# Kernel optimization log

Measured on AMD Instinct MI355X. Metric: run time of the kernel, lower is better.

The kernel has to match this reference:

```python
import jax, jax.numpy as jnp
import numpy as np
import jax.scipy.special as jsp

N_RESERVOIR = 8192
N_INPUT = 64
N_LAYERS = 3
INPUT_SCALE = 0.4
RES_SCALE = 0.9
BIAS_SCALE = 0.1
ALPHA = 1.0  # activation_fn_args = (1.0,)
N_HADAMARD = 1 << int(np.ceil(np.log2(N_INPUT + N_RESERVOIR)))  # 16384
N_PADDING = N_HADAMARD - N_RESERVOIR - N_INPUT
BATCH = 512


def fwht(x):
    """Fast Walsh-Hadamard transform along last axis. x: [B, n], n a power of 2."""
    B, n = x.shape
    h = 1
    while h < n:
        x = x.reshape(B, n // (2 * h), 2, h)
        a = x[:, :, 0, :]
        b = x[:, :, 1, :]
        x = jnp.concatenate([a + b, a - b], axis=-1).reshape(B, n)
        h *= 2
    return x


def leaky_erf(x, state, alpha):
    return (1.0 - alpha) * state + alpha * jsp.erf(x)


def setup_inputs() -> dict:
    key = jax.random.key(0)
    k1, k2, k3, k4 = jax.random.split(key, 4)
    state = jax.random.normal(k1, (BATCH, N_RESERVOIR), dtype=jnp.float32)
    inputs = jax.random.normal(k2, (BATCH, N_INPUT), dtype=jnp.float32)
    bias = BIAS_SCALE * jax.random.normal(k3, (N_RESERVOIR,), dtype=jnp.float32)
    # structured-transform diagonals: random Rademacher signs, one per layer
    diag = jnp.where(jax.random.uniform(k4, (N_LAYERS, N_HADAMARD)) < 0.5, -1.0, 1.0).astype(jnp.float32)
    return {"state": state, "inputs": inputs, "bias": bias, "diag": diag}


def reference(state, inputs, bias, diag):
    B = state.shape[0]
    pad = jnp.zeros((B, N_PADDING), dtype=state.dtype)
    X = jnp.concatenate([RES_SCALE * state, INPUT_SCALE * inputs, pad], axis=1)  # [B, N_HADAMARD]
    for l in range(N_LAYERS):
        X = fwht(X * diag[l])
    z = X[:, :N_RESERVOIR] / N_HADAMARD + bias
    return leaky_erf(z, state, ALPHA)
```

## Files before the change

kernel.cpp:

```cpp
#include <hip/hip_runtime.h>
#include <math.h>

#define NH    16384
#define NRES  8192
#define NINP  64
#define BATCH 512

typedef float v2f __attribute__((ext_vector_type(2)));

__device__ __forceinline__ constexpr int gfold(int v) {
    return ((v >> 5) & 7) ^ ((v >> 8) & 7) ^ ((v >> 11) & 7);
}
__device__ __forceinline__ constexpr int physf(int v) {
    return v ^ (gfold(v) << 2);
}

template <int T>
__device__ __forceinline__ void pstage(v2f X[32]) {
#pragma unroll
    for (int p = 0; p < 32; ++p) {
        if (!(p & T)) {
            v2f A = X[p], B = X[p | T];
            X[p]     = A + B;
            X[p | T] = A - B;
        }
    }
}
__device__ __forceinline__ void vstage0(v2f X[32]) {
#pragma unroll
    for (int p = 0; p < 32; ++p) {
        float a = X[p].x, b = X[p].y;
        X[p].x = a + b;
        X[p].y = a - b;
    }
}

template <int CTRL>
__device__ __forceinline__ float dppf(float v) {
    return __builtin_bit_cast(float,
        __builtin_amdgcn_update_dpp(0, __builtin_bit_cast(int, v), CTRL, 0xF, 0xF, true));
}
template <int CTRL>
__device__ __forceinline__ void dpp_swap(float A, float B, bool odd, float& oA, float& oB) {
    float dA = dppf<CTRL>(A), dB = dppf<CTRL>(B);
    oA = odd ? dB : A;
    oB = odd ? B  : dA;
}
__device__ __forceinline__ void pl16_swap(float& a, float& b) {
    asm("v_permlane16_swap_b32 %0, %1" : "+v"(a), "+v"(b));
}
__device__ __forceinline__ void pl32_swap(float& a, float& b) {
    asm("v_permlane32_swap_b32 %0, %1" : "+v"(a), "+v"(b));
}

__device__ __forceinline__ void shuffle_exchange(v2f X[32], bool odd0, bool odd1) {
#pragma unroll
    for (int p = 0; p < 32; ++p) if (!(p & 2)) {
        float a0, a1, b0, b1;
        dpp_swap<0xB1>(X[p].x, X[p | 2].x, odd0, a0, b0);
        dpp_swap<0xB1>(X[p].y, X[p | 2].y, odd0, a1, b1);
        X[p] = (v2f){a0, a1}; X[p | 2] = (v2f){b0, b1};
    }
#pragma unroll
    for (int p = 0; p < 32; ++p) if (!(p & 4)) {
        float a0, a1, b0, b1;
        dpp_swap<0x4E>(X[p].x, X[p | 4].x, odd1, a0, b0);
        dpp_swap<0x4E>(X[p].y, X[p | 4].y, odd1, a1, b1);
        X[p] = (v2f){a0, a1}; X[p | 4] = (v2f){b0, b1};
    }
#pragma unroll
    for (int p = 0; p < 32; ++p) if (!(p & 8)) {
        float a = X[p].x, b = X[p | 8].x; pl16_swap(a, b); X[p].x = a; X[p | 8].x = b;
        float c = X[p].y, d = X[p | 8].y; pl16_swap(c, d); X[p].y = c; X[p | 8].y = d;
    }
#pragma unroll
    for (int p = 0; p < 32; ++p) if (!(p & 16)) {
        float a = X[p].x, b = X[p | 16].x; pl32_swap(a, b); X[p].x = a; X[p | 16].x = b;
        float c = X[p].y, d = X[p | 16].y; pl32_swap(c, d); X[p].y = c; X[p | 16].y = d;
    }
}

#define WRX(Q, SH) do { _Pragma("unroll") \
    for (int j = 0; j < 16; ++j) \
        lds4[(unsigned)((Q) ^ physf(j << (SH))) >> 2] = \
            make_float4(X[2*j].x, X[2*j].y, X[2*j+1].x, X[2*j+1].y); } while (0)

#define RDX(Q, SH) do { _Pragma("unroll") \
    for (int j = 0; j < 16; ++j) { \
        float4 v = lds4[(unsigned)((Q) ^ physf(j << (SH))) >> 2]; \
        X[2*j]   = (v2f){v.x, v.y}; \
        X[2*j+1] = (v2f){v.z, v.w}; } } while (0)

#define DIAG_MUL(BASEPTR, SH) do { \
    _Pragma("unroll") for (int h = 0; h < 2; ++h) { \
        float4 dv[8]; \
        _Pragma("unroll") for (int k = 0; k < 8; ++k) \
            dv[k] = *(const float4*)((BASEPTR) + ((h * 8 + k) << (SH))); \
        _Pragma("unroll") for (int k = 0; k < 8; ++k) { \
            const int j = h * 8 + k; \
            X[2*j]   *= (v2f){dv[k].x, dv[k].y}; \
            X[2*j+1] *= (v2f){dv[k].z, dv[k].w}; \
        } \
    } } while (0)

__device__ __forceinline__ float erf_fast(float z) {
    float p = z * z;
    float u = z * fmaf(p, 0.10090f, 1.1283793f);
    float e = __builtin_amdgcn_exp2f(u * 2.8853902f);
    float r = __builtin_amdgcn_rcpf(e + 1.0f);
    return fmaf(-2.0f, r, 1.0f);
}


__global__ __launch_bounds__(256, 2) void st_kernel(
    const float* __restrict__ state, const float* __restrict__ inputs,
    const float* __restrict__ bias,  const float* __restrict__ diag,
    float* __restrict__ out)
{
    __shared__ float4 lds4[NH / 4];
    const int t = threadIdx.x;
    const int r = blockIdx.x;
    const int l = t & 63, w = t >> 6;
    const int l01 = l & 3, l23 = (l >> 2) & 3, l45 = (l >> 4) & 3;
    const bool odd0 = (l & 1), odd1 = (l & 2);

    const int bA = (w << 12) | (l23 << 10) | (l45 << 8) | (l01 << 6);
    const int bB = (w << 12) | (l23 << 10) | (l45 << 4) | (l01 << 2);
    const int bC = (w << 8)  | (l23 << 6)  | (l45 << 4) | (l01 << 2);
    const int bD = (l45 << 12) | (l01 << 10) | (w << 8) | (l23 << 6);

    v2f X[32];

    if (t < 128) {
        const float* srow = state + (size_t)r * NRES + bA;
        const float* d0   = diag + bA;
#pragma unroll
        for (int h = 0; h < 2; ++h) {
            float4 sv[8], dv[8];
#pragma unroll
            for (int k = 0; k < 8; ++k) {
                sv[k] = *(const float4*)(srow + 4 * (h * 8 + k));
                dv[k] = *(const float4*)(d0   + 4 * (h * 8 + k));
            }
#pragma unroll
            for (int k = 0; k < 8; ++k) {
                const int j = h * 8 + k;
                X[2*j]   = (v2f){0.9f * sv[k].x * dv[k].x, 0.9f * sv[k].y * dv[k].y};
                X[2*j+1] = (v2f){0.9f * sv[k].z * dv[k].z, 0.9f * sv[k].w * dv[k].w};
            }
        }
    } else if (t == 128) {
        const float* irow = inputs + r * NINP;
        const float* d0   = diag + NRES;
#pragma unroll
        for (int j = 0; j < 16; ++j) {
            float4 v = *(const float4*)(irow + 4 * j);
            float4 d = *(const float4*)(d0 + 4 * j);
            X[2*j]   = (v2f){0.4f * v.x * d.x, 0.4f * v.y * d.y};
            X[2*j+1] = (v2f){0.4f * v.z * d.z, 0.4f * v.w * d.w};
        }
    } else {
#pragma unroll
        for (int p = 0; p < 32; ++p) X[p] = (v2f){0.f, 0.f};
    }

    vstage0(X); pstage<1>(X); pstage<2>(X);
    pstage<4>(X); pstage<8>(X); pstage<16>(X);

    shuffle_exchange(X, odd0, odd1);
    pstage<2>(X); pstage<4>(X); pstage<8>(X); pstage<16>(X);

    { const int Q = physf(bB); WRX(Q, 6); }
    __syncthreads();
    { const int Q = physf(bC); RDX(Q, 10); }
    pstage<2>(X); pstage<4>(X); pstage<8>(X); pstage<16>(X);
    DIAG_MUL(diag + NH + bC, 10);
    vstage0(X); pstage<1>(X);
    pstage<2>(X); pstage<4>(X); pstage<8>(X); pstage<16>(X);

    shuffle_exchange(X, odd0, odd1);
    pstage<2>(X); pstage<4>(X); pstage<8>(X); pstage<16>(X);

    __syncthreads();
    { const int Q = physf(bD); WRX(Q, 2); }
    __syncthreads();
    { const int Q = physf(bB); RDX(Q, 6); }
    pstage<2>(X); pstage<4>(X); pstage<8>(X); pstage<16>(X);
    DIAG_MUL(diag + 2 * NH + bB, 6);
    vstage0(X); pstage<1>(X);
    pstage<2>(X); pstage<4>(X); pstage<8>(X); pstage<16>(X);

    shuffle_exchange(X, odd0, odd1);
    pstage<2>(X); pstage<4>(X); pstage<8>(X); pstage<16>(X);

    __syncthreads();
    { const int Q = physf(bA); WRX(Q, 2); }
    __syncthreads();
    { const int Q = physf(bC); RDX(Q, 10); }
    pstage<2>(X); pstage<4>(X); pstage<8>(X); pstage<16>(X);

    {
        float* orow = out + (size_t)r * NRES;
        const float inv = 1.0f / (float)NH;
#pragma unroll
        for (int j = 0; j < 8; ++j) {
            float4 b = *(const float4*)(bias + bC + (j << 10));
            float4 o;
            o.x = erf_fast(fmaf(X[2*j].x,   inv, b.x));
            o.y = erf_fast(fmaf(X[2*j].y,   inv, b.y));
            o.z = erf_fast(fmaf(X[2*j+1].x, inv, b.z));
            o.w = erf_fast(fmaf(X[2*j+1].y, inv, b.w));
            *(float4*)(orow + bC + (j << 10)) = o;
        }
    }
}

extern "C" void kernel_launch(void* const* d_in, const int* in_sizes, int n_in,
                              void* d_out, int out_size, void* d_ws, size_t ws_size,
                              hipStream_t stream) {
    (void)in_sizes; (void)n_in; (void)out_size; (void)d_ws; (void)ws_size;
    const float* state  = (const float*)d_in[0];
    const float* inputs = (const float*)d_in[1];
    const float* bias   = (const float*)d_in[2];
    const float* diag   = (const float*)d_in[3];
    float* out = (float*)d_out;

    hipLaunchKernelGGL(st_kernel, dim3(BATCH), dim3(256), 0, stream,
                       state, inputs, bias, diag, out);
}
```

Before: 25.10 us.

## Restructure FWHT data mapping with DPP butterflies and prefetched diagonals

Reworks how each thread's 128 elements map onto the Hadamard index bits across the three layers. The DPP select-swap exchanges become direct DPP butterflies that multiply by a per-lane sign and add the neighbour's value, which removes the separate in-register stages that followed. Diagonal and bias loads are issued before the LDS transposes so their latency overlaps the exchange. Barriers become a raw lgkmcnt wait plus s_barrier, and a final permlane32 swap fixes the output order. The cost is more live registers (the prefetch buffer) and new address mappings that must stay bank-conflict free under the XOR swizzle.

```diff
diff --git a/kernel.cpp b/kernel.cpp
--- a/kernel.cpp
+++ b/kernel.cpp
@@ -8,30 +8,25 @@
 
 typedef float v2f __attribute__((ext_vector_type(2)));
 
-__device__ __forceinline__ constexpr int gfold(int v) {
+__device__ __forceinline__ constexpr int gfoldc(int v) {
     return ((v >> 5) & 7) ^ ((v >> 8) & 7) ^ ((v >> 11) & 7);
 }
-__device__ __forceinline__ constexpr int physf(int v) {
-    return v ^ (gfold(v) << 2);
-}
+__device__ __forceinline__ constexpr int physf(int v) { return v ^ (gfoldc(v) << 2); }
 
 template <int T>
 __device__ __forceinline__ void pstage(v2f X[32]) {
 #pragma unroll
-    for (int p = 0; p < 32; ++p) {
-        if (!(p & T)) {
-            v2f A = X[p], B = X[p | T];
-            X[p]     = A + B;
-            X[p | T] = A - B;
-        }
+    for (int p = 0; p < 32; ++p) if (!(p & T)) {
+        v2f A = X[p], B = X[p | T];
+        X[p]     = A + B;
+        X[p | T] = A - B;
     }
 }
 __device__ __forceinline__ void vstage0(v2f X[32]) {
 #pragma unroll
     for (int p = 0; p < 32; ++p) {
         float a = X[p].x, b = X[p].y;
-        X[p].x = a + b;
-        X[p].y = a - b;
+        X[p].x = a + b; X[p].y = a - b;
     }
 }
 
@@ -41,38 +36,29 @@
         __builtin_amdgcn_update_dpp(0, __builtin_bit_cast(int, v), CTRL, 0xF, 0xF, true));
 }
 template <int CTRL>
-__device__ __forceinline__ void dpp_swap(float A, float B, bool odd, float& oA, float& oB) {
-    float dA = dppf<CTRL>(A), dB = dppf<CTRL>(B);
-    oA = odd ? dB : A;
-    oB = odd ? B  : dA;
-}
+__device__ __forceinline__ void dpp_bfly(v2f X[32], v2f sgn) {
+#pragma unroll
+    for (int p = 0; p < 32; ++p) {
+        float y0 = dppf<CTRL>(X[p].x);
+        float y1 = dppf<CTRL>(X[p].y);
+        X[p] = sgn * X[p] + (v2f){y0, y1};
+    }
+}
+
 __device__ __forceinline__ void pl16_swap(float& a, float& b) {
     asm("v_permlane16_swap_b32 %0, %1" : "+v"(a), "+v"(b));
 }
 __device__ __forceinline__ void pl32_swap(float& a, float& b) {
     asm("v_permlane32_swap_b32 %0, %1" : "+v"(a), "+v"(b));
 }
-
-__device__ __forceinline__ void shuffle_exchange(v2f X[32], bool odd0, bool odd1) {
-#pragma unroll
-    for (int p = 0; p < 32; ++p) if (!(p & 2)) {
-        float a0, a1, b0, b1;
-        dpp_swap<0xB1>(X[p].x, X[p | 2].x, odd0, a0, b0);
-        dpp_swap<0xB1>(X[p].y, X[p | 2].y, odd0, a1, b1);
-        X[p] = (v2f){a0, a1}; X[p | 2] = (v2f){b0, b1};
-    }
-#pragma unroll
-    for (int p = 0; p < 32; ++p) if (!(p & 4)) {
-        float a0, a1, b0, b1;
-        dpp_swap<0x4E>(X[p].x, X[p | 4].x, odd1, a0, b0);
-        dpp_swap<0x4E>(X[p].y, X[p | 4].y, odd1, a1, b1);
-        X[p] = (v2f){a0, a1}; X[p | 4] = (v2f){b0, b1};
-    }
+__device__ __forceinline__ void swap_j2_l4(v2f X[32]) {
 #pragma unroll
     for (int p = 0; p < 32; ++p) if (!(p & 8)) {
         float a = X[p].x, b = X[p | 8].x; pl16_swap(a, b); X[p].x = a; X[p | 8].x = b;
         float c = X[p].y, d = X[p | 8].y; pl16_swap(c, d); X[p].y = c; X[p | 8].y = d;
     }
+}
+__device__ __forceinline__ void swap_j3_l5(v2f X[32]) {
 #pragma unroll
     for (int p = 0; p < 32; ++p) if (!(p & 16)) {
         float a = X[p].x, b = X[p | 16].x; pl32_swap(a, b); X[p].x = a; X[p | 16].x = b;
@@ -80,28 +66,36 @@
     }
 }
 
-#define WRX(Q, SH) do { _Pragma("unroll") \
-    for (int j = 0; j < 16; ++j) \
-        lds4[(unsigned)((Q) ^ physf(j << (SH))) >> 2] = \
-            make_float4(X[2*j].x, X[2*j].y, X[2*j+1].x, X[2*j+1].y); } while (0)
-
-#define RDX(Q, SH) do { _Pragma("unroll") \
-    for (int j = 0; j < 16; ++j) { \
-        float4 v = lds4[(unsigned)((Q) ^ physf(j << (SH))) >> 2]; \
-        X[2*j]   = (v2f){v.x, v.y}; \
-        X[2*j+1] = (v2f){v.z, v.w}; } } while (0)
-
-#define DIAG_MUL(BASEPTR, SH) do { \
-    _Pragma("unroll") for (int h = 0; h < 2; ++h) { \
-        float4 dv[8]; \
-        _Pragma("unroll") for (int k = 0; k < 8; ++k) \
-            dv[k] = *(const float4*)((BASEPTR) + ((h * 8 + k) << (SH))); \
-        _Pragma("unroll") for (int k = 0; k < 8; ++k) { \
-            const int j = h * 8 + k; \
-            X[2*j]   *= (v2f){dv[k].x, dv[k].y}; \
-            X[2*j+1] *= (v2f){dv[k].z, dv[k].w}; \
-        } \
+#define GOFF4(g, G0, G1, G2, G3) \
+    ((((g) & 1) ? (G0) : 0) | (((g) & 2) ? (G1) : 0) | \
+     (((g) & 4) ? (G2) : 0) | (((g) & 8) ? (G3) : 0))
+
+#define WRX(Q, G0, G1, G2, G3) do { _Pragma("unroll") \
+    for (int g = 0; g < 16; ++g) { \
+        const int a = (Q) ^ physf(GOFF4(g, G0, G1, G2, G3)); \
+        lds4[(unsigned)a >> 2] = \
+            make_float4(X[2*g].x, X[2*g].y, X[2*g+1].x, X[2*g+1].y); \
     } } while (0)
+
+#define RDX(Q, G0, G1, G2, G3) do { _Pragma("unroll") \
+    for (int g = 0; g < 16; ++g) { \
+        const int a = (Q) ^ physf(GOFF4(g, G0, G1, G2, G3)); \
+        float4 v = lds4[(unsigned)a >> 2]; \
+        X[2*g]   = (v2f){v.x, v.y}; \
+        X[2*g+1] = (v2f){v.z, v.w}; \
+    } } while (0)
+
+#define DIAG_LOAD(PF, BASE, G0, G1, G2, G3) do { _Pragma("unroll") \
+    for (int g = 0; g < 16; ++g) \
+        (PF)[g] = *(const float4*)((BASE) + GOFF4(g, G0, G1, G2, G3)); } while (0)
+
+#define DIAG_APPLY(PF) do { _Pragma("unroll") \
+    for (int g = 0; g < 16; ++g) { \
+        X[2*g]   *= (v2f){(PF)[g].x, (PF)[g].y}; \
+        X[2*g+1] *= (v2f){(PF)[g].z, (PF)[g].w}; \
+    } } while (0)
+
+#define BAR() asm volatile("s_waitcnt lgkmcnt(0)\n\ts_barrier" ::: "memory")
 
 __device__ __forceinline__ float erf_fast(float z) {
     float p = z * z;
@@ -110,7 +104,6 @@
     float r = __builtin_amdgcn_rcpf(e + 1.0f);
     return fmaf(-2.0f, r, 1.0f);
 }
-
 
 __global__ __launch_bounds__(256, 2) void st_kernel(
     const float* __restrict__ state, const float* __restrict__ inputs,
@@ -121,96 +114,118 @@
     const int t = threadIdx.x;
     const int r = blockIdx.x;
     const int l = t & 63, w = t >> 6;
-    const int l01 = l & 3, l23 = (l >> 2) & 3, l45 = (l >> 4) & 3;
-    const bool odd0 = (l & 1), odd1 = (l & 2);
-
-    const int bA = (w << 12) | (l23 << 10) | (l45 << 8) | (l01 << 6);
-    const int bB = (w << 12) | (l23 << 10) | (l45 << 4) | (l01 << 2);
-    const int bC = (w << 8)  | (l23 << 6)  | (l45 << 4) | (l01 << 2);
-    const int bD = (l45 << 12) | (l01 << 10) | (w << 8) | (l23 << 6);
+    const int l0=l&1, l1=(l>>1)&1, l2=(l>>2)&1, l3=(l>>3)&1, l4=(l>>4)&1, l5=(l>>5)&1;
+    const int w0=w&1, w1=(w>>1)&1;
+
+    const v2f s1 = (v2f){l0 ? -1.f : 1.f, l0 ? -1.f : 1.f};
+    const v2f s2 = (v2f){l1 ? -1.f : 1.f, l1 ? -1.f : 1.f};
+
+    const int b_w1 = l0*64 + l1*128 + l2*256 + l3*512 + l4*16  + l5*32
+                   + w0*4096 + w1*8192;
+    const int b_r1 = l0*64 + l1*128 + l2*4   + l3*8   + l4*16  + l5*32
+                   + w0*1024 + w1*2048;
+    const int b_w2 = l0*64 + l1*128 + l2*4   + l3*8   + l4*4096 + l5*8192
+                   + w0*1024 + w1*2048;
+    const int b_r2 = l0*64 + l1*128 + l2*256 + l3*512 + l4*4096 + l5*8192
+                   + w0*16 + w1*32;
+    const int b_w3 = l0*64 + l1*128 + l2*256 + l3*512 + l4*1024 + l5*2048
+                   + w0*16 + w1*32;
+    const int b_r3 = l0*4  + l1*8   + l2*64  + l3*128 + l4*1024 + l5*8192
+                   + w0*2048 + w1*4096;
+    const int b_st = l0*4  + l1*8   + l2*64  + l3*128 + l4*1024 + l5*512
+                   + w0*2048 + w1*4096;
 
     v2f X[32];
+    float4 pf[16];
 
     if (t < 128) {
-        const float* srow = state + (size_t)r * NRES + bA;
-        const float* d0   = diag + bA;
-#pragma unroll
-        for (int h = 0; h < 2; ++h) {
-            float4 sv[8], dv[8];
-#pragma unroll
-            for (int k = 0; k < 8; ++k) {
-                sv[k] = *(const float4*)(srow + 4 * (h * 8 + k));
-                dv[k] = *(const float4*)(d0   + 4 * (h * 8 + k));
-            }
-#pragma unroll
-            for (int k = 0; k < 8; ++k) {
-                const int j = h * 8 + k;
-                X[2*j]   = (v2f){0.9f * sv[k].x * dv[k].x, 0.9f * sv[k].y * dv[k].y};
-                X[2*j+1] = (v2f){0.9f * sv[k].z * dv[k].z, 0.9f * sv[k].w * dv[k].w};
-            }
+        const float* srow = state + (size_t)r * NRES + t * 64;
+        const float* d0   = diag + t * 64;
+#pragma unroll
+        for (int g = 0; g < 16; ++g) {
+            float4 v = *(const float4*)(srow + 4 * g);
+            float4 d = *(const float4*)(d0 + 4 * g);
+            X[2*g]   = (v2f){0.9f * v.x * d.x, 0.9f * v.y * d.y};
+            X[2*g+1] = (v2f){0.9f * v.z * d.z, 0.9f * v.w * d.w};
         }
     } else if (t == 128) {
         const float* irow = inputs + r * NINP;
         const float* d0   = diag + NRES;
 #pragma unroll
-        for (int j = 0; j < 16; ++j) {
-            float4 v = *(const float4*)(irow + 4 * j);
-            float4 d = *(const float4*)(d0 + 4 * j);
-            X[2*j]   = (v2f){0.4f * v.x * d.x, 0.4f * v.y * d.y};
-            X[2*j+1] = (v2f){0.4f * v.z * d.z, 0.4f * v.w * d.w};
+        for (int g = 0; g < 16; ++g) {
+            float4 v = *(const float4*)(irow + 4 * g);
+            float4 d = *(const float4*)(d0 + 4 * g);
+            X[2*g]   = (v2f){0.4f * v.x * d.x, 0.4f * v.y * d.y};
+            X[2*g+1] = (v2f){0.4f * v.z * d.z, 0.4f * v.w * d.w};
         }
     } else {
 #pragma unroll
         for (int p = 0; p < 32; ++p) X[p] = (v2f){0.f, 0.f};
     }
 
-    vstage0(X); pstage<1>(X); pstage<2>(X);
-    pstage<4>(X); pstage<8>(X); pstage<16>(X);
-
-    shuffle_exchange(X, odd0, odd1);
-    pstage<2>(X); pstage<4>(X); pstage<8>(X); pstage<16>(X);
-
-    { const int Q = physf(bB); WRX(Q, 6); }
-    __syncthreads();
-    { const int Q = physf(bC); RDX(Q, 10); }
-    pstage<2>(X); pstage<4>(X); pstage<8>(X); pstage<16>(X);
-    DIAG_MUL(diag + NH + bC, 10);
     vstage0(X); pstage<1>(X);
     pstage<2>(X); pstage<4>(X); pstage<8>(X); pstage<16>(X);
-
-    shuffle_exchange(X, odd0, odd1);
-    pstage<2>(X); pstage<4>(X); pstage<8>(X); pstage<16>(X);
-
-    __syncthreads();
-    { const int Q = physf(bD); WRX(Q, 2); }
-    __syncthreads();
-    { const int Q = physf(bB); RDX(Q, 6); }
-    pstage<2>(X); pstage<4>(X); pstage<8>(X); pstage<16>(X);
-    DIAG_MUL(diag + 2 * NH + bB, 6);
+    dpp_bfly<0xB1>(X, s1);
+    dpp_bfly<0x4E>(X, s2);
+    swap_j2_l4(X); swap_j3_l5(X);
+    pstage<8>(X); pstage<16>(X);
+
+    DIAG_LOAD(pf, diag + NH + b_r1, 256, 512, 4096, 8192);
+
+    { const int Q = physf(b_w1); WRX(Q, 4, 8, 1024, 2048); }
+    BAR();
+    { const int Q = physf(b_r1); RDX(Q, 256, 512, 4096, 8192); }
+    pstage<2>(X); pstage<4>(X); pstage<8>(X); pstage<16>(X);
+
+    DIAG_APPLY(pf);
     vstage0(X); pstage<1>(X);
     pstage<2>(X); pstage<4>(X); pstage<8>(X); pstage<16>(X);
-
-    shuffle_exchange(X, odd0, odd1);
-    pstage<2>(X); pstage<4>(X); pstage<8>(X); pstage<16>(X);
-
-    __syncthreads();
-    { const int Q = physf(bA); WRX(Q, 2); }
-    __syncthreads();
-    { const int Q = physf(bC); RDX(Q, 10); }
-    pstage<2>(X); pstage<4>(X); pstage<8>(X); pstage<16>(X);
+    dpp_bfly<0xB1>(X, s1);
+    dpp_bfly<0x4E>(X, s2);
+    swap_j2_l4(X); swap_j3_l5(X);
+    pstage<8>(X); pstage<16>(X);
+
+    DIAG_LOAD(pf, diag + 2 * NH + b_r2, 4, 8, 1024, 2048);
+
+    BAR();
+    { const int Q = physf(b_w2); WRX(Q, 256, 512, 16, 32); }
+    BAR();
+    { const int Q = physf(b_r2); RDX(Q, 4, 8, 1024, 2048); }
+    pstage<2>(X); pstage<4>(X); pstage<8>(X); pstage<16>(X);
+
+    DIAG_APPLY(pf);
+    vstage0(X); pstage<1>(X);
+    pstage<2>(X); pstage<4>(X); pstage<8>(X); pstage<16>(X);
+    dpp_bfly<0xB1>(X, s1);
+    dpp_bfly<0x4E>(X, s2);
+    swap_j2_l4(X); swap_j3_l5(X);
+    pstage<8>(X); pstage<16>(X);
+
+    float4 bv[8];
+#pragma unroll
+    for (int g = 0; g < 8; ++g)
+        bv[g] = *(const float4*)(bias + b_st + GOFF4(g, 16, 32, 256, 0));
+
+    BAR();
+    { const int Q = physf(b_w3); WRX(Q, 4, 8, 4096, 8192); }
+    BAR();
+    { const int Q = physf(b_r3); RDX(Q, 16, 32, 256, 512); }
+    pstage<2>(X); pstage<4>(X); pstage<8>(X); pstage<16>(X);
+
+    swap_j3_l5(X);
 
     {
         float* orow = out + (size_t)r * NRES;
         const float inv = 1.0f / (float)NH;
 #pragma unroll
-        for (int j = 0; j < 8; ++j) {
-            float4 b = *(const float4*)(bias + bC + (j << 10));
+        for (int g = 0; g < 8; ++g) {
+            const int a = b_st + GOFF4(g, 16, 32, 256, 0);
             float4 o;
-            o.x = erf_fast(fmaf(X[2*j].x,   inv, b.x));
-            o.y = erf_fast(fmaf(X[2*j].y,   inv, b.y));
-            o.z = erf_fast(fmaf(X[2*j+1].x, inv, b.z));
-            o.w = erf_fast(fmaf(X[2*j+1].y, inv, b.w));
-            *(float4*)(orow + bC + (j << 10)) = o;
+            o.x = erf_fast(fmaf(X[2*g].x,   inv, bv[g].x));
+            o.y = erf_fast(fmaf(X[2*g].y,   inv, bv[g].y));
+            o.z = erf_fast(fmaf(X[2*g+1].x, inv, bv[g].z));
+            o.w = erf_fast(fmaf(X[2*g+1].y, inv, bv[g].w));
+            *(float4*)(orow + a) = o;
         }
     }
 }
```

Measured after the change: 24.79 us. No clear change (-1.2%).
